# Kernel optimization log

Measured on AMD Instinct MI355X. Metric: run time of the kernel, lower is better.

Reference implementation:

```python
import jax, jax.numpy as jnp
from jax import lax
import numpy as np

D_MODEL = 512
H = 4
DK = 128
DV = 256
DFF = 2048
N_LAYERS = 12
N_LOC = 100  # 10x10 patches

CONV_SPECS = [(8, 3, 3), (16, 8, 3), (32, 16, 3), (32, 32, 3), (64, 32, 3),
              (64, 64, 3), (128, 64, 3), (128, 128, 3), (256, 128, 3), (512, 256, 2)]
RELU_AFTER = [False, True, False, True, True, True, True, True, True, False]


def setup_inputs() -> dict:
    key = jax.random.key(0)
    keys = iter(jax.random.split(key, 64))

    def nrm(shape, scale=0.02):
        return jax.random.normal(next(keys), shape, dtype=jnp.float32) * scale

    inp = {"x": jax.random.normal(next(keys), (1, 3, 200, 200), dtype=jnp.float32)}
    for i, (o, c, k) in enumerate(CONV_SPECS, 1):
        inp[f"cw{i}"] = nrm((o, c, k, k))
        inp[f"cb{i}"] = nrm((o,))
    inp["Wq"] = nrm((N_LAYERS, H, D_MODEL, DK))
    inp["Wk"] = nrm((N_LAYERS, H, D_MODEL, DK))
    inp["Wv"] = nrm((N_LAYERS, H, D_MODEL, DV))
    inp["Wo"] = nrm((N_LAYERS, H * DV, D_MODEL))
    inp["W1"] = nrm((N_LAYERS, D_MODEL, DFF))
    inp["b1"] = nrm((N_LAYERS, DFF))
    inp["W2"] = nrm((N_LAYERS, DFF, D_MODEL))
    inp["b2"] = nrm((N_LAYERS, D_MODEL))
    return inp


def _extract_patches(x):
    # x: [1,3,200,200] -> 100 patches of [3,20,20], index = i*10 + j
    # patch(i,j) = x[:, :, 20j:20(j+1), 20i:20(i+1)]  (i=cols outer, j=rows inner)
    x = x.reshape(3, 10, 20, 10, 20)            # [c, j_blk, row, i_blk, col]
    return jnp.transpose(x, (3, 1, 0, 2, 4)).reshape(N_LOC, 3, 20, 20)


def _local_embed(patches, cws, cbs):
    h = patches  # [100,3,20,20]
    for w, b, r in zip(cws, cbs, RELU_AFTER):
        h = lax.conv_general_dilated(h, w, (1, 1), 'VALID',
                                     dimension_numbers=('NCHW', 'OIHW', 'NCHW'))
        h = h + b[None, :, None, None]
        if r:
            h = jax.nn.relu(h)
    return h.reshape(N_LOC, D_MODEL)  # spatial reduced to 1x1


def _location_embeddings():
    # createLocationEmbedding(i, j) only uses i (the column-block coordinate).
    pos = jnp.repeat(jnp.arange(0, 200, 20, dtype=jnp.float32), 10)  # [100]
    k = jnp.arange(256, dtype=jnp.float32)
    inv = jnp.power(jnp.float32(10000.0), 2.0 * k / 256.0)
    ang = pos[:, None] / inv[None, :]  # [100,256]
    return jnp.concatenate([jnp.sin(ang), jnp.cos(ang)], axis=1)  # [100,512]


def _encoder_layer(h, Wq, Wk, Wv, Wo, W1, b1, W2, b2):
    # Multi-head attention; NOTE: scale uses K.size(0) = n_locations (faithful quirk).
    scale = 1.0 / jnp.sqrt(jnp.float32(N_LOC))
    q = jnp.einsum('nd,hdk->hnk', h, Wq)
    k = jnp.einsum('nd,hdk->hnk', h, Wk)
    v = jnp.einsum('nd,hdv->hnv', h, Wv)
    s = jnp.einsum('hnk,hmk->hnm', q, k) * scale
    a = jax.nn.softmax(s, axis=-1)
    o = jnp.einsum('hnm,hmv->hnv', a, v)
    o = jnp.transpose(o, (1, 0, 2)).reshape(N_LOC, H * DV)
    h = h + o @ Wo
    h = h + (jax.nn.relu(h @ W1 + b1) @ W2 + b2)
    return h


def reference(x, cw1, cb1, cw2, cb2, cw3, cb3, cw4, cb4, cw5, cb5,
              cw6, cb6, cw7, cb7, cw8, cb8, cw9, cb9, cw10, cb10,
              Wq, Wk, Wv, Wo, W1, b1, W2, b2):
    cws = [cw1, cw2, cw3, cw4, cw5, cw6, cw7, cw8, cw9, cw10]
    cbs = [cb1, cb2, cb3, cb4, cb5, cb6, cb7, cb8, cb9, cb10]
    patches = _extract_patches(x)
    h = _local_embed(patches, cws, cbs)
    h = h + _location_embeddings()
    for n in range(N_LAYERS):
        h = _encoder_layer(h, Wq[n], Wk[n], Wv[n], Wo[n], W1[n], b1[n], W2[n], b2[n])
    return h
```

## Files before the change

### kernel.cpp

```cpp
#include <hip/hip_runtime.h>
#include <math.h>

#define NLOC 100

typedef __attribute__((ext_vector_type(8))) _Float16 half8;
typedef __attribute__((ext_vector_type(4))) float f32x4;

#define XP_OFF    0
#define H_OFF     160000
#define QKV_OFF   211200
#define OCAT_OFF  416000
#define FFN_OFF   467200
#define ACTA_OFF  569600
#define ACTB_OFF  889664
#define CWH_OFF   1209728
#define CW1_OFF   1765504
#define WQKVT_OFF 1765824
#define WOT_OFF   8057280
#define W1T_OFF   11203008
#define W2T_OFF   17494464

struct WPack { const float* w[9]; };

__global__ __launch_bounds__(256) void stage_xp(const float* __restrict__ x, float* __restrict__ xp)
{
    int idx = blockIdx.x*256 + threadIdx.x;
    if (idx >= 160000) return;
    int c = idx & 3;
    int idx2 = idx >> 2;
    int p = idx2 / 400;
    int rr = idx2 - p*400;
    int y = rr / 20, xx = rr - y*20;
    int pi = p/10, pj = p - pi*10;
    float v = 0.f;
    if (c < 3) v = x[c*40000 + (pj*20 + y)*200 + pi*20 + xx];
    xp[idx] = v;
}

__global__ __launch_bounds__(256) void cw1repack(const float* __restrict__ w, float* __restrict__ w4)
{
    int idx = threadIdx.x;
    if (idx >= 288) return;
    int c = idx & 3;
    int r = idx >> 2;
    int oc = r / 9, kk = r - oc*9;
    int ky = kk/3, kx = kk - ky*3;
    float v = 0.f;
    if (c < 3) v = w[((oc*3 + c)*3 + ky)*3 + kx];
    w4[idx] = v;
}

__global__ __launch_bounds__(256) void cwrepack(WPack wp, unsigned short* __restrict__ dst)
{
    const int Cin[9]  = {8,16,32,32,64,64,128,128,256};
    const int shift[9]= {3,4,5,5,6,6,7,7,8};
    const int KS[9]   = {3,3,3,3,3,3,3,3,2};
    const int Kpad[9] = {96,160,288,288,576,576,1152,1152,1024};
    const int off[10] = {0,1536,6656,15872,34304,71168,144896,292352,587264,1111552};
    const int total = 1111552;
    for (int i = blockIdx.x*blockDim.x + threadIdx.x; i < total; i += gridDim.x*blockDim.x) {
        int l = 0;
        while (i >= off[l+1]) ++l;
        int rem = i - off[l];
        int kp = Kpad[l];
        int oc = rem / kp;
        int k  = rem - oc*kp;
        int ci = Cin[l];
        int ic = k & (ci - 1);
        int kk = k >> shift[l];
        int ks = KS[l], k2 = ks*ks;
        float v = 0.f;
        if (kk < k2) {
            int ky = kk / ks, kx = kk - ky*ks;
            v = wp.w[l][((oc*ci + ic)*ks + ky)*ks + kx];
        }
        _Float16 hv = (_Float16)v;
        dst[i] = __builtin_bit_cast(unsigned short, hv);
    }
}

__global__ __launch_bounds__(256) void conv1k(const float4* __restrict__ xp4,
    const float4* __restrict__ w4, const float* __restrict__ bias, unsigned short* __restrict__ out)
{
    int idx = blockIdx.x*256 + threadIdx.x;
    if (idx >= 259200) return;
    int oc = idx & 7;
    int r = idx >> 3;
    int p = r / 324;
    int s = r - p*324;
    int sy = s / 18, sx = s - sy*18;
    const float4* ip = xp4 + (size_t)(p*20 + sy)*20 + sx;
    float acc = 0.f;
    #pragma unroll
    for (int ky = 0; ky < 3; ++ky)
        #pragma unroll
        for (int kx = 0; kx < 3; ++kx) {
            float4 iv = ip[ky*20 + kx];
            float4 wv = w4[oc*9 + ky*3 + kx];
            acc += iv.x*wv.x + iv.y*wv.y + iv.z*wv.z;
        }
    acc += bias[oc];
    _Float16 hv = (_Float16)acc;
    out[idx] = __builtin_bit_cast(unsigned short, hv);
}

template<int CIN, int COUT, int KS, int HIN, int WIN, int HOUT, int WOUT, int KPAD, int RELU, int LAST>
__global__ __launch_bounds__(256) void convM(const unsigned short* __restrict__ in,
    const unsigned short* __restrict__ wth, const float* __restrict__ bias,
    unsigned short* __restrict__ out, float* __restrict__ hout)
{
    constexpr int HW = HOUT*WOUT;
    constexpr int M = 100*HW;
    constexpr int MT = (M + 15)/16;
    constexpr int NT = COUT/16;
    int wave = threadIdx.x >> 6, lane = threadIdx.x & 63;
    int t = blockIdx.x*4 + wave;
    if (t >= MT*NT) return;
    int mt = t % MT, nt = t / MT;
    int mrow = lane & 15, quad = lane >> 4;
    int mg = mt*16 + mrow; if (mg >= M) mg = M - 1;
    int p = mg / HW, s = mg - p*HW;
    int sy = s / WOUT, sx = s - sy*WOUT;
    const unsigned short* ap = in + ((size_t)((p*HIN + sy)*WIN + sx))*CIN;
    const unsigned short* bp = wth + ((size_t)(nt*16 + mrow))*KPAD + quad*8;
    f32x4 acc = {0.f, 0.f, 0.f, 0.f};
    #pragma unroll
    for (int k0 = 0; k0 < KPAD; k0 += 32) {
        int k = k0 + quad*8;
        int kk = k / CIN; if (kk > KS*KS - 1) kk = KS*KS - 1;
        int ky = kk / KS, kx = kk - ky*KS;
        uint4 av = *(const uint4*)(ap + (ky*WIN + kx)*CIN + (k & (CIN-1)));
        uint4 bv = *(const uint4*)(bp + k0);
        acc = __builtin_amdgcn_mfma_f32_16x16x32_f16(
            __builtin_bit_cast(half8, av), __builtin_bit_cast(half8, bv), acc, 0, 0, 0);
    }
    int n = nt*16 + mrow;
    float bv = bias[n];
    #pragma unroll
    for (int r = 0; r < 4; ++r) {
        int m = mt*16 + quad*4 + r;
        if (m < M) {
            float v = acc[r] + bv;
            if (RELU) v = fmaxf(v, 0.f);
            if (LAST) {
                int pi = m / 10;
                float pos = 20.f * (float)pi;
                int dd = n & 255;
                float inv = powf(10000.f, (float)dd * (1.f/128.f));
                float ang = pos / inv;
                v += (n < 256) ? sinf(ang) : cosf(ang);
                hout[(size_t)m*512 + n] = v;
            } else {
                _Float16 hv = (_Float16)v;
                out[(size_t)m*COUT + n] = __builtin_bit_cast(unsigned short, hv);
            }
        }
    }
}

__global__ __launch_bounds__(256) void wtrans(
    const float* __restrict__ src, unsigned short* __restrict__ dst,
    int K, int N, int matsPerLayer, int dstLayerStride, int dstBase)
{
    __shared__ float t[32][33];
    int mz = blockIdx.z;
    int layer = mz / matsPerLayer;
    int mi = mz - layer*matsPerLayer;
    const float* s = src + (size_t)mz * K * N;
    unsigned short* d = dst + (size_t)layer*dstLayerStride + dstBase + (size_t)mi * N * K;
    int n0 = blockIdx.x*32, k0 = blockIdx.y*32;
    int tx = threadIdx.x & 31, ty = threadIdx.x >> 5;
    #pragma unroll
    for (int i = 0; i < 32; i += 8) t[ty + i][tx] = s[(size_t)(k0 + ty + i)*N + n0 + tx];
    __syncthreads();
    #pragma unroll
    for (int i = 0; i < 32; i += 8) {
        _Float16 hv = (_Float16)t[tx][ty + i];
        d[(size_t)(n0 + ty + i)*K + k0 + tx] = __builtin_bit_cast(unsigned short, hv);
    }
}

template<int ABITS, int RELU, int ATOMIC, int STOREH>
__global__ __launch_bounds__(256) void gemm16(
    const void* __restrict__ Av, int lda,
    const unsigned short* __restrict__ Bt, int K,
    const float* __restrict__ bias,
    float* __restrict__ C, unsigned short* __restrict__ Ch, int ldc,
    int kchunk)
{
    int lane = threadIdx.x & 63;
    int wave = threadIdx.x >> 6;
    int mrow = lane & 15, quad = lane >> 4;
    int n0 = blockIdx.x*64 + wave*16;
    int m0 = blockIdx.y*16;
    int arow = m0 + mrow; if (arow > 99) arow = 99;
    int k0 = blockIdx.z * kchunk;
    const unsigned short* bp = Bt + (size_t)(n0 + mrow)*K + quad*8 + k0;
    f32x4 acc = {0.f, 0.f, 0.f, 0.f};
    if (ABITS == 16) {
        const unsigned short* ap = (const unsigned short*)Av + (size_t)arow*lda + quad*8 + k0;
        for (int k = 0; k < kchunk; k += 32) {
            uint4 au = *(const uint4*)(ap + k);
            uint4 bu = *(const uint4*)(bp + k);
            acc = __builtin_amdgcn_mfma_f32_16x16x32_f16(
                __builtin_bit_cast(half8, au), __builtin_bit_cast(half8, bu), acc, 0, 0, 0);
        }
    } else {
        const float* ap = (const float*)Av + (size_t)arow*lda + quad*8 + k0;
        for (int k = 0; k < kchunk; k += 32) {
            float4 f0 = *(const float4*)(ap + k);
            float4 f1 = *(const float4*)(ap + k + 4);
            half8 af;
            af[0] = (_Float16)f0.x; af[1] = (_Float16)f0.y;
            af[2] = (_Float16)f0.z; af[3] = (_Float16)f0.w;
            af[4] = (_Float16)f1.x; af[5] = (_Float16)f1.y;
            af[6] = (_Float16)f1.z; af[7] = (_Float16)f1.w;
            uint4 bu = *(const uint4*)(bp + k);
            acc = __builtin_amdgcn_mfma_f32_16x16x32_f16(
                af, __builtin_bit_cast(half8, bu), acc, 0, 0, 0);
        }
    }
    int n = n0 + mrow;
    float bv = (bias != nullptr && blockIdx.z == 0) ? bias[n] : 0.f;
    #pragma unroll
    for (int r = 0; r < 4; ++r) {
        int row = m0 + quad*4 + r;
        if (row < 100) {
            float v = acc[r] + bv;
            if (RELU) v = fmaxf(v, 0.f);
            if (ATOMIC) atomicAdd(&C[(size_t)row*ldc + n], v);
            else if (C != nullptr) C[(size_t)row*ldc + n] = v;
            if (STOREH) {
                _Float16 hv = (_Float16)v;
                Ch[(size_t)row*ldc + n] = __builtin_bit_cast(unsigned short, hv);
            }
        }
    }
}

__global__ __launch_bounds__(256) void attn_kernel(
    const float* __restrict__ qkv, unsigned short* __restrict__ ocat)
{
    __shared__ float qr[128];
    __shared__ float p[100];
    __shared__ float red[2];
    int bx = blockIdx.x;
    int hh = bx / 100, nn = bx - hh*100;
    int t = threadIdx.x;
    if (t < 128) qr[t] = qkv[(size_t)nn*2048 + hh*128 + t];
    __syncthreads();
    float sv = 0.f;
    if (t < 100) {
        const float4* kp = (const float4*)(qkv + (size_t)t*2048 + 512 + hh*128);
        const float4* q4 = (const float4*)qr;
        float s0=0.f, s1=0.f, s2=0.f, s3=0.f;
        #pragma unroll 8
        for (int j = 0; j < 32; ++j) {
            float4 a = q4[j], b = kp[j];
            s0 += a.x*b.x; s1 += a.y*b.y; s2 += a.z*b.z; s3 += a.w*b.w;
        }
        sv = (s0+s1+s2+s3) * 0.1f;
        p[t] = sv;
    }
    __syncthreads();
    if (t < 64) {
        float m = fmaxf(p[t], (t+64 < 100) ? p[t+64] : -1e30f);
        for (int o = 32; o > 0; o >>= 1) m = fmaxf(m, __shfl_down(m, o));
        if (t == 0) red[0] = m;
    }
    __syncthreads();
    float mx = red[0];
    if (t < 100) p[t] = expf(sv - mx);
    __syncthreads();
    if (t < 64) {
        float s = p[t] + ((t+64 < 100) ? p[t+64] : 0.f);
        for (int o = 32; o > 0; o >>= 1) s += __shfl_down(s, o);
        if (t == 0) red[1] = s;
    }
    __syncthreads();
    float inv = 1.0f / red[1];
    const float* vp = qkv + 1024 + hh*256 + t;
    float acc = 0.f;
    #pragma unroll 4
    for (int m = 0; m < 100; ++m) acc += p[m] * vp[(size_t)m*2048];
    _Float16 hv = (_Float16)(acc * inv);
    ocat[(size_t)nn*1024 + hh*256 + t] = __builtin_bit_cast(unsigned short, hv);
}

__global__ __launch_bounds__(256) void copyk(const float* __restrict__ s, float* __restrict__ d, int n)
{
    int i = blockIdx.x*256 + threadIdx.x;
    if (i < n) d[i] = s[i];
}

extern "C" void kernel_launch(void* const* d_in, const int* in_sizes, int n_in,
                              void* d_out, int out_size, void* d_ws, size_t ws_size,
                              hipStream_t stream)
{
    const float* x = (const float*)d_in[0];
    const float* cw1 = (const float*)d_in[1];
    const float* cb[10];
    WPack wpk;
    for (int i = 0; i < 10; ++i) cb[i] = (const float*)d_in[2 + 2*i];
    for (int i = 0; i < 9; ++i)  wpk.w[i] = (const float*)d_in[3 + 2*i];
    const float* Wq = (const float*)d_in[21];
    const float* Wk = (const float*)d_in[22];
    const float* Wv = (const float*)d_in[23];
    const float* Wo = (const float*)d_in[24];
    const float* W1 = (const float*)d_in[25];
    const float* b1 = (const float*)d_in[26];
    const float* W2 = (const float*)d_in[27];
    const float* b2 = (const float*)d_in[28];

    float* ws = (float*)d_ws;
    float* xp  = ws + XP_OFF;
    float* h   = ws + H_OFF;
    float* qkv = ws + QKV_OFF;
    unsigned short* ocat = (unsigned short*)(ws + OCAT_OFF);
    unsigned short* ffn  = (unsigned short*)(ws + FFN_OFF);
    unsigned short* aA   = (unsigned short*)(ws + ACTA_OFF);
    unsigned short* aB   = (unsigned short*)(ws + ACTB_OFF);
    unsigned short* cwh  = (unsigned short*)(ws + CWH_OFF);
    float* cw14 = ws + CW1_OFF;
    unsigned short* wqkvt = (unsigned short*)(ws + WQKVT_OFF);
    unsigned short* wot   = (unsigned short*)(ws + WOT_OFF);
    unsigned short* w1t   = (unsigned short*)(ws + W1T_OFF);
    unsigned short* w2t   = (unsigned short*)(ws + W2T_OFF);

    cw1repack<<<2, 256, 0, stream>>>(cw1, cw14);
    cwrepack<<<2172, 256, 0, stream>>>(wpk, cwh);
    wtrans<<<dim3(4, 16, 48),  256, 0, stream>>>(Wq, wqkvt, 512, 128,  4, 2048*512, 0);
    wtrans<<<dim3(4, 16, 48),  256, 0, stream>>>(Wk, wqkvt, 512, 128,  4, 2048*512, 512*512);
    wtrans<<<dim3(8, 16, 48),  256, 0, stream>>>(Wv, wqkvt, 512, 256,  4, 2048*512, 1024*512);
    wtrans<<<dim3(16, 32, 12), 256, 0, stream>>>(Wo, wot,  1024, 512,  1, 512*1024, 0);
    wtrans<<<dim3(64, 16, 12), 256, 0, stream>>>(W1, w1t,   512, 2048, 1, 2048*512, 0);
    wtrans<<<dim3(16, 64, 12), 256, 0, stream>>>(W2, w2t,  2048, 512,  1, 512*2048, 0);

    stage_xp<<<625, 256, 0, stream>>>(x, xp);
    conv1k<<<1013, 256, 0, stream>>>((const float4*)xp, (const float4*)cw14, cb[0], aA);
    convM<8,  16, 3,18,18,16,16,  96,1,0><<<400, 256, 0, stream>>>(aA, cwh + 0,      cb[1], aB, nullptr);
    convM<16, 32, 3,16,16,14,14, 160,0,0><<<613, 256, 0, stream>>>(aB, cwh + 1536,   cb[2], aA, nullptr);
    convM<32, 32, 3,14,14,12,12, 288,1,0><<<450, 256, 0, stream>>>(aA, cwh + 6656,   cb[3], aB, nullptr);
    convM<32, 64, 3,12,12,10,10, 288,1,0><<<625, 256, 0, stream>>>(aB, cwh + 15872,  cb[4], aA, nullptr);
    convM<64, 64, 3,10,10, 8, 8, 576,1,0><<<400, 256, 0, stream>>>(aA, cwh + 34304,  cb[5], aB, nullptr);
    convM<64,128, 3, 8, 8, 6, 6, 576,1,0><<<450, 256, 0, stream>>>(aB, cwh + 71168,  cb[6], aA, nullptr);
    convM<128,128,3, 6, 6, 4, 4,1152,1,0><<<200, 256, 0, stream>>>(aA, cwh + 144896, cb[7], aB, nullptr);
    convM<128,256,3, 4, 4, 2, 2,1152,1,0><<<100, 256, 0, stream>>>(aB, cwh + 292352, cb[8], aA, nullptr);
    convM<256,512,2, 2, 2, 1, 1,1024,0,1><<<56,  256, 0, stream>>>(aA, cwh + 587264, cb[9], nullptr, h);

    for (int n = 0; n < 12; ++n) {
        const unsigned short* Bq  = wqkvt + (size_t)n * 2048 * 512;
        const unsigned short* Bo  = wot   + (size_t)n * 512 * 1024;
        const unsigned short* Bf1 = w1t   + (size_t)n * 2048 * 512;
        const unsigned short* Bf2 = w2t   + (size_t)n * 512 * 2048;
        gemm16<32,0,0,0><<<dim3(32, 7, 1), 256, 0, stream>>>(h, 512, Bq, 512,
            nullptr, qkv, nullptr, 2048, 512);
        attn_kernel<<<400, 256, 0, stream>>>(qkv, ocat);
        gemm16<16,0,1,0><<<dim3(8, 7, 4), 256, 0, stream>>>(ocat, 1024, Bo, 1024,
            nullptr, h, nullptr, 512, 256);
        gemm16<32,1,0,1><<<dim3(32, 7, 1), 256, 0, stream>>>(h, 512, Bf1, 512,
            b1 + (size_t)n*2048, nullptr, ffn, 2048, 512);
        gemm16<16,0,1,0><<<dim3(8, 7, 8), 256, 0, stream>>>(ffn, 2048, Bf2, 2048,
            b2 + (size_t)n*512, h, nullptr, 512, 256);
    }
    copyk<<<200, 256, 0, stream>>>(h, (float*)d_out, NLOC*512);
}
```

Before: 880.8 us.

## Fuse whole pipeline into one cooperative persistent megakernel with grid syncs

Replaces the sequence of many small kernel launches (repacks, ten convs, and five kernels per encoder layer) with a single cooperative kernel of 256 workgroups. Stages are separated by grid-wide barriers, and work is distributed over waves with strided tile loops. This removes per-launch overhead and launch gaps across roughly 70 launches. In exchange it adds about 70 grid barriers and fixes the GEMM tiling at 16x16 tiles per wave, which may lose efficiency compared with the tuned separate kernels. The old launch path is kept as a fallback when cooperative launch is unavailable.

```diff
diff --git a/kernel.cpp b/kernel.cpp
--- a/kernel.cpp
+++ b/kernel.cpp
@@ -1,5 +1,8 @@
 #include <hip/hip_runtime.h>
+#include <hip/hip_cooperative_groups.h>
 #include <math.h>
+
+namespace cg = cooperative_groups;
 
 #define NLOC 100
 
@@ -20,7 +23,373 @@
 #define W1T_OFF   11203008
 #define W2T_OFF   17494464
 
+#define NWG  256
+#define NTHR 512
+
 struct WPack { const float* w[9]; };
+
+struct KParams {
+    const float* x;
+    const float* cw1;
+    WPack wpk;
+    const float* cb0; const float* cb1; const float* cb2; const float* cb3; const float* cb4;
+    const float* cb5; const float* cb6; const float* cb7; const float* cb8; const float* cb9;
+    const float* Wq; const float* Wk; const float* Wv; const float* Wo;
+    const float* W1; const float* b1; const float* W2; const float* b2;
+    float* ws;
+    float* out;
+};
+
+struct TJob {
+    const float* src; unsigned short* dst;
+    int K, N, mpl, lstride, base, tiles;
+};
+
+
+template<int CIN, int COUT, int KS, int HIN, int WIN, int HOUT, int WOUT, int KPAD, int RELU, int LAST>
+__device__ __forceinline__ void convM_dev(const unsigned short* __restrict__ in,
+    const unsigned short* __restrict__ wth, const float* __restrict__ bias,
+    unsigned short* __restrict__ out, float* __restrict__ hout,
+    int gwave, int nwaves, int lane)
+{
+    constexpr int HW = HOUT*WOUT;
+    constexpr int M = 100*HW;
+    constexpr int MT = (M + 15)/16;
+    constexpr int NT = COUT/16;
+    const int mrow = lane & 15, quad = lane >> 4;
+    for (int t = gwave; t < MT*NT; t += nwaves) {
+        int mt = t % MT, nt = t / MT;
+        int mg = mt*16 + mrow; if (mg >= M) mg = M - 1;
+        int p = mg / HW, s = mg - p*HW;
+        int sy = s / WOUT, sx = s - sy*WOUT;
+        const unsigned short* ap = in + ((size_t)((p*HIN + sy)*WIN + sx))*CIN;
+        const unsigned short* bp = wth + ((size_t)(nt*16 + mrow))*KPAD + quad*8;
+        f32x4 acc = {0.f, 0.f, 0.f, 0.f};
+        #pragma unroll 4
+        for (int k0 = 0; k0 < KPAD; k0 += 32) {
+            int k = k0 + quad*8;
+            int kk = k / CIN; if (kk > KS*KS - 1) kk = KS*KS - 1;
+            int ky = kk / KS, kx = kk - ky*KS;
+            uint4 av = *(const uint4*)(ap + (ky*WIN + kx)*CIN + (k & (CIN-1)));
+            uint4 bv = *(const uint4*)(bp + k0);
+            acc = __builtin_amdgcn_mfma_f32_16x16x32_f16(
+                __builtin_bit_cast(half8, av), __builtin_bit_cast(half8, bv), acc, 0, 0, 0);
+        }
+        int n = nt*16 + mrow;
+        float bvv = bias[n];
+        #pragma unroll
+        for (int r = 0; r < 4; ++r) {
+            int m = mt*16 + quad*4 + r;
+            if (m < M) {
+                float v = acc[r] + bvv;
+                if (RELU) v = fmaxf(v, 0.f);
+                if (LAST) {
+                    int pi = m / 10;
+                    float pos = 20.f * (float)pi;
+                    int dd = n & 255;
+                    float inv = powf(10000.f, (float)dd * (1.f/128.f));
+                    float ang = pos / inv;
+                    v += (n < 256) ? sinf(ang) : cosf(ang);
+                    hout[(size_t)m*512 + n] = v;
+                } else {
+                    _Float16 hv = (_Float16)v;
+                    out[(size_t)m*COUT + n] = __builtin_bit_cast(unsigned short, hv);
+                }
+            }
+        }
+    }
+}
+
+template<int ABITS, int RELU, int RESID, int OUTH>
+__device__ __forceinline__ void gemm_dev(const void* __restrict__ Av, int lda,
+    const unsigned short* __restrict__ Bt, int K, int N,
+    const float* __restrict__ bias, float* __restrict__ C, unsigned short* __restrict__ Ch,
+    int ldc, int gwave, int nwaves, int lane)
+{
+    const int NT = N >> 4;
+    const int tiles = 7*NT;
+    const int mrow = lane & 15, quad = lane >> 4;
+    for (int t = gwave; t < tiles; t += nwaves) {
+        const int mt = t % 7, nt = t / 7;
+        int arow = mt*16 + mrow; if (arow > 99) arow = 99;
+        const unsigned short* bp = Bt + (size_t)(nt*16 + mrow)*K + quad*8;
+        f32x4 acc = {0.f, 0.f, 0.f, 0.f};
+        if (ABITS == 16) {
+            const unsigned short* ap = (const unsigned short*)Av + (size_t)arow*lda + quad*8;
+            #pragma unroll 4
+            for (int k = 0; k < K; k += 32) {
+                uint4 au = *(const uint4*)(ap + k);
+                uint4 bu = *(const uint4*)(bp + k);
+                acc = __builtin_amdgcn_mfma_f32_16x16x32_f16(
+                    __builtin_bit_cast(half8, au), __builtin_bit_cast(half8, bu), acc, 0, 0, 0);
+            }
+        } else {
+            const float* ap = (const float*)Av + (size_t)arow*lda + quad*8;
+            #pragma unroll 4
+            for (int k = 0; k < K; k += 32) {
+                float4 f0 = *(const float4*)(ap + k);
+                float4 f1 = *(const float4*)(ap + k + 4);
+                half8 af;
+                af[0] = (_Float16)f0.x; af[1] = (_Float16)f0.y;
+                af[2] = (_Float16)f0.z; af[3] = (_Float16)f0.w;
+                af[4] = (_Float16)f1.x; af[5] = (_Float16)f1.y;
+                af[6] = (_Float16)f1.z; af[7] = (_Float16)f1.w;
+                uint4 bu = *(const uint4*)(bp + k);
+                acc = __builtin_amdgcn_mfma_f32_16x16x32_f16(
+                    af, __builtin_bit_cast(half8, bu), acc, 0, 0, 0);
+            }
+        }
+        const int n = nt*16 + mrow;
+        const float bv = (bias != nullptr) ? bias[n] : 0.f;
+        #pragma unroll
+        for (int r = 0; r < 4; ++r) {
+            int row = mt*16 + quad*4 + r;
+            if (row < 100) {
+                float v = acc[r] + bv;
+                if (RELU) v = fmaxf(v, 0.f);
+                if (RESID) v += C[(size_t)row*ldc + n];
+                if (!OUTH) {
+                    C[(size_t)row*ldc + n] = v;
+                } else {
+                    _Float16 hv = (_Float16)v;
+                    Ch[(size_t)row*ldc + n] = __builtin_bit_cast(unsigned short, hv);
+                }
+            }
+        }
+    }
+}
+
+__device__ __forceinline__ void attn_dev(const float* __restrict__ qkv,
+    unsigned short* __restrict__ ocat, int wg, int tid, float* sh)
+{
+    const int half = tid >> 8;
+    const int t = tid & 255;
+    float* qr  = sh + half*128;
+    float* pp  = sh + 256 + half*128;
+    float* red = sh + 512 + half*2;
+    if (wg < 200) {
+        const int u = wg*2 + half;
+        const int hh = u / 100, nn = u - hh*100;
+        if (t < 128) qr[t] = qkv[(size_t)nn*2048 + hh*128 + t];
+        __syncthreads();
+        float sv = 0.f;
+        if (t < 100) {
+            const float4* kp = (const float4*)(qkv + (size_t)t*2048 + 512 + hh*128);
+            const float4* q4 = (const float4*)qr;
+            float s0=0.f, s1=0.f, s2=0.f, s3=0.f;
+            #pragma unroll 8
+            for (int j = 0; j < 32; ++j) {
+                float4 a = q4[j], b = kp[j];
+                s0 += a.x*b.x; s1 += a.y*b.y; s2 += a.z*b.z; s3 += a.w*b.w;
+            }
+            sv = (s0+s1+s2+s3) * 0.1f;
+            pp[t] = sv;
+        }
+        __syncthreads();
+        if (t < 64) {
+            float m = fmaxf(pp[t], (t+64 < 100) ? pp[t+64] : -1e30f);
+            for (int o = 32; o > 0; o >>= 1) m = fmaxf(m, __shfl_down(m, o));
+            if (t == 0) red[0] = m;
+        }
+        __syncthreads();
+        float mx = red[0];
+        if (t < 100) pp[t] = expf(sv - mx);
+        __syncthreads();
+        if (t < 64) {
+            float ssum = pp[t] + ((t+64 < 100) ? pp[t+64] : 0.f);
+            for (int o = 32; o > 0; o >>= 1) ssum += __shfl_down(ssum, o);
+            if (t == 0) red[1] = ssum;
+        }
+        __syncthreads();
+        float inv = 1.0f / red[1];
+        const float* vp = qkv + 1024 + hh*256 + t;
+        float acc = 0.f;
+        #pragma unroll 4
+        for (int m = 0; m < 100; ++m) acc += pp[m] * vp[(size_t)m*2048];
+        _Float16 hv = (_Float16)(acc * inv);
+        ocat[(size_t)nn*1024 + hh*256 + t] = __builtin_bit_cast(unsigned short, hv);
+    }
+}
+
+__global__ __launch_bounds__(NTHR) void megakernel(KParams P)
+{
+    cg::grid_group grid = cg::this_grid();
+    const int tid = threadIdx.x;
+    const int wg  = blockIdx.x;
+    const int gthread = wg*NTHR + tid;
+    constexpr int nthreads = NWG*NTHR;
+    const int gwave = gthread >> 6;
+    constexpr int nwaves = nthreads >> 6;
+    const int lane = tid & 63;
+
+    float* ws = P.ws;
+    float* xp   = ws + XP_OFF;
+    float* hbuf = ws + H_OFF;
+    float* qkv  = ws + QKV_OFF;
+    unsigned short* ocat = (unsigned short*)(ws + OCAT_OFF);
+    unsigned short* ffnb = (unsigned short*)(ws + FFN_OFF);
+    unsigned short* aA   = (unsigned short*)(ws + ACTA_OFF);
+    unsigned short* aB   = (unsigned short*)(ws + ACTB_OFF);
+    unsigned short* cwh  = (unsigned short*)(ws + CWH_OFF);
+    float* cw14 = ws + CW1_OFF;
+    unsigned short* wqkvt = (unsigned short*)(ws + WQKVT_OFF);
+    unsigned short* wot   = (unsigned short*)(ws + WOT_OFF);
+    unsigned short* w1t   = (unsigned short*)(ws + W1T_OFF);
+    unsigned short* w2t   = (unsigned short*)(ws + W2T_OFF);
+
+    __shared__ TJob jobs[6];
+    __shared__ float sh[516];
+
+    if (tid == 0) {
+        jobs[0] = TJob{P.Wq, wqkvt,  512,  128, 4, 2048*512, 0,        1536};
+        jobs[1] = TJob{P.Wk, wqkvt,  512,  128, 4, 2048*512, 512*512,  1536};
+        jobs[2] = TJob{P.Wv, wqkvt,  512,  256, 4, 2048*512, 1024*512, 3072};
+        jobs[3] = TJob{P.Wo, wot,   1024,  512, 1, 512*1024, 0,        3072};
+        jobs[4] = TJob{P.W1, w1t,    512, 2048, 1, 2048*512, 0,        6144};
+        jobs[5] = TJob{P.W2, w2t,   2048,  512, 1, 512*2048, 0,        6144};
+    }
+    __syncthreads();
+
+    for (int idx = gthread; idx < 160000; idx += nthreads) {
+        int c = idx & 3;
+        int idx2 = idx >> 2;
+        int p = idx2 / 400;
+        int rr = idx2 - p*400;
+        int y = rr / 20, xx = rr - y*20;
+        int pi = p/10, pj = p - pi*10;
+        float v = 0.f;
+        if (c < 3) v = P.x[c*40000 + (pj*20 + y)*200 + pi*20 + xx];
+        xp[idx] = v;
+    }
+    if (gthread < 288) {
+        int c = gthread & 3;
+        int r = gthread >> 2;
+        int oc = r / 9, kk = r - oc*9;
+        int ky = kk/3, kx = kk - ky*3;
+        float v = 0.f;
+        if (c < 3) v = P.cw1[((oc*3 + c)*3 + ky)*3 + kx];
+        cw14[gthread] = v;
+    }
+    {
+        const int Cin[9]   = {8,16,32,32,64,64,128,128,256};
+        const int shiftv[9]= {3,4,5,5,6,6,7,7,8};
+        const int KSa[9]   = {3,3,3,3,3,3,3,3,2};
+        const int Kpad[9]  = {96,160,288,288,576,576,1152,1152,1024};
+        const int off[10]  = {0,1536,6656,15872,34304,71168,144896,292352,587264,1111552};
+        for (int i = gthread; i < 1111552; i += nthreads) {
+            int l = 0;
+            while (i >= off[l+1]) ++l;
+            int rem = i - off[l];
+            int kp = Kpad[l];
+            int oc = rem / kp;
+            int k  = rem - oc*kp;
+            int ci = Cin[l];
+            int ic = k & (ci - 1);
+            int kk = k >> shiftv[l];
+            int ks = KSa[l], k2 = ks*ks;
+            float v = 0.f;
+            if (kk < k2) {
+                int ky = kk / ks, kx = kk - ky*ks;
+                v = P.wpk.w[l][((oc*ci + ic)*ks + ky)*ks + kx];
+            }
+            _Float16 hv = (_Float16)v;
+            cwh[i] = __builtin_bit_cast(unsigned short, hv);
+        }
+    }
+    for (int t = gwave; t < 21504; t += nwaves) {
+        int j = 0, rem = t;
+        while (rem >= jobs[j].tiles) { rem -= jobs[j].tiles; ++j; }
+        const int K = jobs[j].K, N = jobs[j].N;
+        const int nb = N >> 6, kb = K >> 5;
+        int mat = rem / (nb*kb);
+        int r2  = rem - mat*(nb*kb);
+        int n0  = (r2 % nb) << 6;
+        int k0  = (r2 / nb) << 5;
+        const float* s = jobs[j].src + (size_t)mat*K*N;
+        int layer = mat / jobs[j].mpl, mi = mat - layer*jobs[j].mpl;
+        unsigned short* d = jobs[j].dst + (size_t)layer*jobs[j].lstride + jobs[j].base + (size_t)mi*N*K;
+        int nn = n0 + lane;
+        float v[32];
+        #pragma unroll
+        for (int kk = 0; kk < 32; ++kk) v[kk] = s[(size_t)(k0+kk)*N + nn];
+        unsigned int u[16];
+        #pragma unroll
+        for (int q = 0; q < 16; ++q) {
+            _Float16 a = (_Float16)v[2*q], b = (_Float16)v[2*q+1];
+            u[q] = (unsigned int)__builtin_bit_cast(unsigned short, a)
+                 | ((unsigned int)__builtin_bit_cast(unsigned short, b) << 16);
+        }
+        uint4* dp = (uint4*)(d + (size_t)nn*K + k0);
+        dp[0] = make_uint4(u[0],u[1],u[2],u[3]);
+        dp[1] = make_uint4(u[4],u[5],u[6],u[7]);
+        dp[2] = make_uint4(u[8],u[9],u[10],u[11]);
+        dp[3] = make_uint4(u[12],u[13],u[14],u[15]);
+    }
+
+    grid.sync();
+
+    for (int idx = gthread; idx < 259200; idx += nthreads) {
+        int oc = idx & 7;
+        int r = idx >> 3;
+        int p = r / 324;
+        int s = r - p*324;
+        int sy = s / 18, sx = s - sy*18;
+        const float4* ip = (const float4*)xp + (size_t)(p*20 + sy)*20 + sx;
+        const float4* w4 = (const float4*)cw14;
+        float acc = 0.f;
+        #pragma unroll
+        for (int ky = 0; ky < 3; ++ky)
+            #pragma unroll
+            for (int kx = 0; kx < 3; ++kx) {
+                float4 iv = ip[ky*20 + kx];
+                float4 wv = w4[oc*9 + ky*3 + kx];
+                acc += iv.x*wv.x + iv.y*wv.y + iv.z*wv.z;
+            }
+        acc += P.cb0[oc];
+        _Float16 hv = (_Float16)acc;
+        aA[idx] = __builtin_bit_cast(unsigned short, hv);
+    }
+    grid.sync();
+
+    convM_dev<8,  16, 3,18,18,16,16,  96,1,0>(aA, cwh + 0,      P.cb1, aB, nullptr, gwave, nwaves, lane);
+    grid.sync();
+    convM_dev<16, 32, 3,16,16,14,14, 160,0,0>(aB, cwh + 1536,   P.cb2, aA, nullptr, gwave, nwaves, lane);
+    grid.sync();
+    convM_dev<32, 32, 3,14,14,12,12, 288,1,0>(aA, cwh + 6656,   P.cb3, aB, nullptr, gwave, nwaves, lane);
+    grid.sync();
+    convM_dev<32, 64, 3,12,12,10,10, 288,1,0>(aB, cwh + 15872,  P.cb4, aA, nullptr, gwave, nwaves, lane);
+    grid.sync();
+    convM_dev<64, 64, 3,10,10, 8, 8, 576,1,0>(aA, cwh + 34304,  P.cb5, aB, nullptr, gwave, nwaves, lane);
+    grid.sync();
+    convM_dev<64,128, 3, 8, 8, 6, 6, 576,1,0>(aB, cwh + 71168,  P.cb6, aA, nullptr, gwave, nwaves, lane);
+    grid.sync();
+    convM_dev<128,128,3, 6, 6, 4, 4,1152,1,0>(aA, cwh + 144896, P.cb7, aB, nullptr, gwave, nwaves, lane);
+    grid.sync();
+    convM_dev<128,256,3, 4, 4, 2, 2,1152,1,0>(aB, cwh + 292352, P.cb8, aA, nullptr, gwave, nwaves, lane);
+    grid.sync();
+    convM_dev<256,512,2, 2, 2, 1, 1,1024,0,1>(aA, cwh + 587264, P.cb9, nullptr, hbuf, gwave, nwaves, lane);
+    grid.sync();
+
+    for (int ln = 0; ln < 12; ++ln) {
+        const unsigned short* Bq  = wqkvt + (size_t)ln * (2048*512);
+        const unsigned short* Bo  = wot   + (size_t)ln * (512*1024);
+        const unsigned short* Bf1 = w1t   + (size_t)ln * (2048*512);
+        const unsigned short* Bf2 = w2t   + (size_t)ln * (512*2048);
+        gemm_dev<32,0,0,0>(hbuf, 512, Bq, 512, 2048, nullptr, qkv, nullptr, 2048, gwave, nwaves, lane);
+        grid.sync();
+        attn_dev(qkv, ocat, wg, tid, sh);
+        grid.sync();
+        gemm_dev<16,0,1,0>(ocat, 1024, Bo, 1024, 512, nullptr, hbuf, nullptr, 512, gwave, nwaves, lane);
+        grid.sync();
+        gemm_dev<32,1,0,1>(hbuf, 512, Bf1, 512, 2048, P.b1 + (size_t)ln*2048, nullptr, ffnb, 2048, gwave, nwaves, lane);
+        grid.sync();
+        gemm_dev<16,0,1,0>(ffnb, 2048, Bf2, 2048, 512, P.b2 + (size_t)ln*512, hbuf, nullptr, 512, gwave, nwaves, lane);
+        grid.sync();
+    }
+
+    for (int i = gthread; i < 51200; i += nthreads) P.out[i] = hbuf[i];
+}
+
 
 __global__ __launch_bounds__(256) void stage_xp(const float* __restrict__ x, float* __restrict__ xp)
 {
@@ -293,9 +662,7 @@
     if (i < n) d[i] = s[i];
 }
 
-extern "C" void kernel_launch(void* const* d_in, const int* in_sizes, int n_in,
-                              void* d_out, int out_size, void* d_ws, size_t ws_size,
-                              hipStream_t stream)
+static void launch_fallback(void* const* d_in, void* d_out, void* d_ws, hipStream_t stream)
 {
     const float* x = (const float*)d_in[0];
     const float* cw1 = (const float*)d_in[1];
@@ -365,3 +732,41 @@
     }
     copyk<<<200, 256, 0, stream>>>(h, (float*)d_out, NLOC*512);
 }
+
+extern "C" void kernel_launch(void* const* d_in, const int* in_sizes, int n_in,
+                              void* d_out, int out_size, void* d_ws, size_t ws_size,
+                              hipStream_t stream)
+{
+    KParams P;
+    P.x   = (const float*)d_in[0];
+    P.cw1 = (const float*)d_in[1];
+    const float* cbs[10];
+    for (int i = 0; i < 10; ++i) cbs[i] = (const float*)d_in[2 + 2*i];
+    for (int i = 0; i < 9; ++i)  P.wpk.w[i] = (const float*)d_in[3 + 2*i];
+    P.cb0 = cbs[0]; P.cb1 = cbs[1]; P.cb2 = cbs[2]; P.cb3 = cbs[3]; P.cb4 = cbs[4];
+    P.cb5 = cbs[5]; P.cb6 = cbs[6]; P.cb7 = cbs[7]; P.cb8 = cbs[8]; P.cb9 = cbs[9];
+    P.Wq = (const float*)d_in[21];
+    P.Wk = (const float*)d_in[22];
+    P.Wv = (const float*)d_in[23];
+    P.Wo = (const float*)d_in[24];
+    P.W1 = (const float*)d_in[25];
+    P.b1 = (const float*)d_in[26];
+    P.W2 = (const float*)d_in[27];
+    P.b2 = (const float*)d_in[28];
+    P.ws  = (float*)d_ws;
+    P.out = (float*)d_out;
+
+    static int coop = -1;
+    if (coop < 0) {
+        int v = 0;
+        if (hipDeviceGetAttribute(&v, hipDeviceAttributeCooperativeLaunch, 0) != hipSuccess) v = 0;
+        coop = v;
+    }
+    if (coop) {
+        void* args[] = { (void*)&P };
+        hipError_t e = hipLaunchCooperativeKernel((const void*)megakernel,
+                                                  dim3(NWG), dim3(NTHR), (void**)args, 0, stream);
+        if (e == hipSuccess) return;
+    }
+    launch_fallback(d_in, d_out, d_ws, stream);
+}
```

Measured after the change: 3.272 ms. 3.71x slower.
